# Kernel tuning notes

Hardware: AMD Instinct MI355X
Metric: run time of the kernel (lower is better)

Reference implementation:

```python
import jax, jax.numpy as jnp
import numpy as np

# ---- geometry constants (match init_kwargs) ----
A3, A2, W2D = 180, 128, 384          # cone views, parallel angles, 2D sino detector bins
NV, NU = 192, 256                    # cone detector rows/cols (== 2D BP recon grid)
VZ, VY, VX = 192, 192, 192           # volume shape
DS2D = 2.0                           # 2D sinogram detector spacing
DU, DV = 2.0, 2.0                    # cone detector spacing
VOX = 1.0                            # voxel spacing
DSO, DSD = 750.0, 1200.0             # source-isocenter / source-detector distance


def _grad_last(x):
    """torch.gradient along last axis with unit spacing (central diff, one-sided edges)."""
    left = x[..., 1:2] - x[..., 0:1]
    mid = (x[..., 2:] - x[..., :-2]) * 0.5
    right = x[..., -1:] - x[..., -2:-1]
    return jnp.concatenate([left, mid, right], axis=-1)


def _parallel_bp_2d(sino):
    """Batched 2D parallel-beam backprojection. sino [A3, A2, W2D] -> [A3, NV, NU]."""
    dt = sino.dtype
    thetas = jnp.arange(A2, dtype=dt) * jnp.asarray(np.pi / A2, dt)
    ys = (jnp.arange(NV, dtype=dt) - (NV - 1) / 2.0) * DV   # recon grid = detector plane
    xs = (jnp.arange(NU, dtype=dt) - (NU - 1) / 2.0) * DU
    Yg, Xg = ys[:, None], xs[None, :]

    def body(acc, inp):
        th, s_a = inp                       # s_a: [A3, W2D] (one angle, all views)
        pos = (Xg * jnp.cos(th) + Yg * jnp.sin(th)) / DS2D + (W2D - 1) / 2.0  # [NV,NU]
        i0 = jnp.floor(pos).astype(jnp.int32)
        f = (pos - i0).astype(dt)
        i1 = i0 + 1
        w0 = (1.0 - f) * ((i0 >= 0) & (i0 < W2D)).astype(dt)
        w1 = f * ((i1 >= 0) & (i1 < W2D)).astype(dt)
        i0c = jnp.clip(i0, 0, W2D - 1)
        i1c = jnp.clip(i1, 0, W2D - 1)
        g = s_a[:, i0c] * w0 + s_a[:, i1c] * w1   # [A3, NV, NU]
        return acc + g, None

    acc = jnp.zeros((A3, NV, NU), dt)
    acc, _ = jax.lax.scan(jax.checkpoint(body), acc, (thetas, jnp.swapaxes(sino, 0, 1)))
    return acc * jnp.asarray(np.pi / A2, dt)


def _weights_3d(dt):
    """Cosine detector weight D / sqrt(D^2 + u^2 + v^2), shape [NV, NU]."""
    us = (jnp.arange(NU, dtype=dt) - (NU - 1) / 2.0) * DU
    vs = (jnp.arange(NV, dtype=dt) - (NV - 1) / 2.0) * DV
    return DSD / jnp.sqrt(DSD * DSD + us[None, :] ** 2 + vs[:, None] ** 2)


def _cone_bp_3d(proj):
    """Circular cone-beam backprojection. proj [A3, NV, NU] -> [VZ, VY, VX]."""
    dt = proj.dtype
    betas = jnp.arange(A3, dtype=dt) * jnp.asarray(2.0 * np.pi / A3, dt)
    zs = (jnp.arange(VZ, dtype=dt) - (VZ - 1) / 2.0) * VOX
    ys = (jnp.arange(VY, dtype=dt) - (VY - 1) / 2.0) * VOX
    xs = (jnp.arange(VX, dtype=dt) - (VX - 1) / 2.0) * VOX
    Z, Y, X = zs[:, None, None], ys[None, :, None], xs[None, None, :]

    def body(acc, inp):
        beta, p = inp                                     # p: [NV, NU]
        cb, sb = jnp.cos(beta), jnp.sin(beta)
        r = X * cb + Y * sb                               # toward source
        t = -X * sb + Y * cb                              # detector u direction
        denom = DSO - r                                   # [1,VY,VX] (broadcast)
        iu = (DSD * t / denom) / DU + (NU - 1) / 2.0      # [1,VY,VX]
        iv = (DSD * Z / denom) / DV + (NV - 1) / 2.0      # [VZ,VY,VX]
        i0u = jnp.floor(iu).astype(jnp.int32); fu = (iu - i0u).astype(dt); i1u = i0u + 1
        i0v = jnp.floor(iv).astype(jnp.int32); fv = (iv - i0v).astype(dt); i1v = i0v + 1
        inb = lambda i, n: ((i >= 0) & (i < n)).astype(dt)
        m0u, m1u = inb(i0u, NU), inb(i1u, NU)
        m0v, m1v = inb(i0v, NV), inb(i1v, NV)
        i0uc, i1uc = jnp.clip(i0u, 0, NU - 1), jnp.clip(i1u, 0, NU - 1)
        i0vc, i1vc = jnp.clip(i0v, 0, NV - 1), jnp.clip(i1v, 0, NV - 1)
        val = (p[i0vc, i0uc] * ((1 - fv) * m0v) * ((1 - fu) * m0u)
               + p[i0vc, i1uc] * ((1 - fv) * m0v) * (fu * m1u)
               + p[i1vc, i0uc] * (fv * m1v) * ((1 - fu) * m0u)
               + p[i1vc, i1uc] * (fv * m1v) * (fu * m1u))   # [VZ,VY,VX]
        w = (DSO / denom) ** 2                              # FDK distance weight
        return acc + w * val, None

    acc = jnp.zeros((VZ, VY, VX), dt)
    acc, _ = jax.lax.scan(jax.checkpoint(body), acc, (betas, proj))
    return acc * jnp.asarray(2.0 * np.pi / A3, dt)


def setup_inputs() -> dict:
    key = jax.random.key(0)
    k1, k2 = jax.random.split(key)
    sinogram = jax.random.normal(k1, (1, 1, A3, A2, W2D), dtype=jnp.float32)
    weight_init = jax.random.uniform(k2, (A3, A2, W2D), dtype=jnp.float32)
    return {"sinogram": sinogram, "weight_init": weight_init}


def reference(sinogram, weight_init):
    ws = sinogram[0] * weight_init          # [1, A3, A2, W2D]
    d = _grad_last(ws)[0]                   # gradient along dim=3, squeeze dim 0
    cb = _parallel_bp_2d(d)                 # [A3, NV, NU]
    wcb = cb * _weights_3d(cb.dtype)        # Defrise-Clack detector weighting
    reco = _cone_bp_3d(wcb)                 # [VZ, VY, VX]
    return reco[None]                       # [1, VZ, VY, VX]
```

## Files before the change

kernel.cpp:

```cpp
#include <hip/hip_runtime.h>

#define A3 180
#define A2 128
#define W2D 384
#define NV 192
#define NU 256
#define VZ 192
#define VY 192
#define VX 192

#define BX 32
#define BY 8
#define CZPT 12
#define WROWS 32
#define WDW 64

#define BU2 32
#define BV2 32
#define VPT2 4
#define PW 64

static constexpr double PI_D = 3.14159265358979323846;

typedef float f32x2 __attribute__((ext_vector_type(2)));

#define GLOAD16(gaddr, laddr)                                                    \
    __builtin_amdgcn_global_load_lds(                                            \
        (const __attribute__((address_space(1))) unsigned int*)(gaddr),          \
        (__attribute__((address_space(3))) unsigned int*)(laddr), 16, 0, 0)
#define GLOAD4(gaddr, laddr)                                                     \
    __builtin_amdgcn_global_load_lds(                                            \
        (const __attribute__((address_space(1))) unsigned int*)(gaddr),          \
        (__attribute__((address_space(3))) unsigned int*)(laddr), 4, 0, 0)

__global__ void tables_kernel(float* __restrict__ c2, float* __restrict__ s2,
                              float* __restrict__ cbt, float* __restrict__ sbt) {
    int i = threadIdx.x;
    if (i < A2) {
        float th = (float)i * (float)(PI_D / A2);
        c2[i] = cosf(th);
        s2[i] = sinf(th);
    }
    if (i < A3) {
        float be = (float)i * (float)(2.0 * PI_D / A3);
        cbt[i] = cosf(be);
        sbt[i] = sinf(be);
    }
}

__global__ __launch_bounds__(W2D) void grad_kernel(const float* __restrict__ sino,
                                                   const float* __restrict__ wini,
                                                   float* __restrict__ d) {
    __shared__ float p[W2D];
    size_t base = (size_t)blockIdx.x * W2D;
    int w = threadIdx.x;
    p[w] = sino[base + w] * wini[base + w];
    __syncthreads();
    float g;
    if (w == 0)            g = p[1] - p[0];
    else if (w == W2D - 1) g = p[W2D - 1] - p[W2D - 2];
    else                   g = (p[w + 1] - p[w - 1]) * 0.5f;
    d[base + w] = g;
}

__global__ __launch_bounds__(256) void bp2d_kernel(const float* __restrict__ d,
                                                   const float* __restrict__ c2,
                                                   const float* __restrict__ s2,
                                                   float* __restrict__ wcb) {
    __shared__ float rowwin[2][4][PW];
    __shared__ float csl[A2], ssl[A2];
    __shared__ int umin_s[A2];

    int tid = threadIdx.x;
    int ul = tid & 31;
    int vth = tid >> 5;
    int wv = tid >> 6;
    int lane = tid & 63;
    int u0g = blockIdx.x * BU2;
    int v0g = blockIdx.y * BV2;
    int a3 = blockIdx.z;

    float uf = (float)(u0g + ul) - 127.5f;
    float vf0 = (float)(v0g + vth * VPT2) - 95.5f;
    const float* slab = d + (size_t)a3 * (A2 * W2D);

    if (tid < A2) {
        float c = c2[tid], s = s2[tid];
        csl[tid] = c; ssl[tid] = s;
        float cu0 = ((float)u0g - 127.5f) * c;
        float cu1 = ((float)(u0g + BU2 - 1) - 127.5f) * c;
        float cv0 = ((float)v0g - 95.5f) * s;
        float cv1 = ((float)(v0g + BV2 - 1) - 95.5f) * s;
        float m = fminf(cu0, cu1) + fminf(cv0, cv1) + 191.5f;
        umin_s[tid] = (int)m - 2;
    }
    __syncthreads();

    {
        int um = umin_s[wv];
        int colg = min(um + lane, W2D - 1);
        GLOAD4(slab + wv * W2D + colg, &rowwin[0][wv][0]);
    }
    __syncthreads();

    float acc[VPT2];
#pragma unroll
    for (int k = 0; k < VPT2; ++k) acc[k] = 0.0f;

    for (int g = 0; g < A2 / 4; ++g) {
        int buf = g & 1;
        if (g + 1 < A2 / 4) {
            int aa = (g + 1) * 4 + wv;
            int um = umin_s[aa];
            int colg = min(um + lane, W2D - 1);
            GLOAD4(slab + aa * W2D + colg, &rowwin[buf ^ 1][wv][0]);
        }
#pragma unroll
        for (int j = 0; j < 4; ++j) {
            int aa = g * 4 + j;
            float c = csl[aa], s = ssl[aa];
            float pb = fmaf(uf, c, fmaf(vf0, s, 191.5f - (float)umin_s[aa]));
            const float* rw = rowwin[buf][j];
#pragma unroll
            for (int k = 0; k < VPT2; ++k) {
                float pos = fmaf((float)k, s, pb);
                int i0 = (int)pos;
                float f = __builtin_amdgcn_fractf(pos);
                float r0 = rw[i0], r1 = rw[i0 + 1];
                acc[k] = fmaf(f, r1 - r0, acc[k] + r0);
            }
        }
        __syncthreads();
    }

    float x = uf * 2.0f;
    float scale = (float)((PI_D / A2) * (2.0 * PI_D / A3));
#pragma unroll
    for (int k = 0; k < VPT2; ++k) {
        float y = (vf0 + (float)k) * 2.0f;
        float w3 = 1200.0f * __builtin_amdgcn_rsqf(1440000.0f + x * x + y * y);
        int v = v0g + vth * VPT2 + k;
        wcb[((size_t)a3 * NV + v) * NU + u0g + ul] = acc[k] * scale * w3;
    }
}

__global__ __launch_bounds__(256, 8) void conebp_kernel(const float* __restrict__ wcb,
                                                        const float* __restrict__ cbt,
                                                        const float* __restrict__ sbt,
                                                        float* __restrict__ out) {
    __shared__ float win[2][WROWS * WDW];
    __shared__ int orgs_s[A3 + 2];

    int tid = threadIdx.x;
    int tx = tid & (BX - 1);
    int ty = tid >> 5;
    int wid = tid >> 6;
    int lane = tid & 63;

    int x = blockIdx.x * BX + tx;
    int y = blockIdx.y * BY + ty;
    int z0 = blockIdx.z * CZPT;

    float xf = (float)x - 95.5f;
    float yf = (float)y - 95.5f;
    float z0f = (float)z0 - 95.5f;

    {
        float cxf0 = (float)(blockIdx.x * BX) - 95.5f;
        float cxf1 = cxf0 + (float)(BX - 1);
        float cyf0 = (float)(blockIdx.y * BY) - 95.5f;
        float cyf1 = cyf0 + (float)(BY - 1);
        if (tid < A3) {
            float cbb = cbt[tid], sbb = sbt[tid];
            float iumin = 1e30f, ivmin = 1e30f;
#pragma unroll
            for (int c = 0; c < 4; ++c) {
                float cx = (c & 1) ? cxf1 : cxf0;
                float cy = (c & 2) ? cyf1 : cyf0;
                float rr = cx * cbb + cy * sbb;
                float inv = __builtin_amdgcn_rcpf(750.0f - rr);
                float tt = cy * cbb - cx * sbb;
                iumin = fminf(iumin, fmaf(600.0f * tt, inv, 135.5f));
                ivmin = fminf(ivmin, fmaf(600.0f * z0f, inv, 95.5f));
            }
            int um = (int)iumin - 9;
            um = min(max(um, 0), 192) & ~3;
            int vm = min(max((int)ivmin - 1, 1), 160);
            orgs_s[tid] = (vm << 16) | um;
        }
        if (tid >= A3 && tid < A3 + 2) orgs_s[tid] = (1 << 16);
    }
    __syncthreads();

    f32x2 acc2[CZPT];
#pragma unroll
    for (int k = 0; k < CZPT; ++k) acc2[k] = (f32x2)0.0f;

    unsigned pre = ((unsigned)(lane >> 4) << 8) + ((unsigned)(lane & 15) << 2)
                 + ((unsigned)wid << 10);
    float* const win0 = &win[0][0];
    float* const win1 = &win[1][0];

    int orgc = orgs_s[0];
    int orgn = orgs_s[1];
    {
        unsigned umin = orgc & 0xffffu, vmin = (unsigned)orgc >> 16;
        const float* src = wcb + (vmin << 8) + umin + pre;
        float* dst = win0 + ((unsigned)wid << 8);
        GLOAD16(src, dst);
        GLOAD16(src + 4096, dst + 1024);
    }
    __syncthreads();

    for (int a = 0; a < A3; ++a) {
        int cur = a & 1;

        if (a + 1 < A3) {
            unsigned umin = orgn & 0xffffu, vmin = (unsigned)orgn >> 16;
            const float* src = wcb + (size_t)(a + 1) * (NV * NU)
                             + (vmin << 8) + umin + pre;
            float* dst = (cur ? win0 : win1) + ((unsigned)wid << 8);
            GLOAD16(src, dst);
            GLOAD16(src + 4096, dst + 1024);
        }

        float cb = cbt[a], sb = sbt[a];
        float r = fmaf(xf, cb, yf * sb);
        float t = fmaf(yf, cb, -xf * sb);
        float inv = __builtin_amdgcn_rcpf(750.0f - r);
        float iub = fmaf(600.0f * t, inv, 135.5f);
        int u0 = (int)iub - 8;
        float fu = __builtin_amdgcn_fractf(iub);
        float wgt = 750.0f * inv;
        wgt *= wgt;
        float wa = ((unsigned)u0 < NU) ? (1.0f - fu) * wgt : 0.0f;
        float wb = ((unsigned)(u0 + 1) < NU) ? fu * wgt : 0.0f;
        f32x2 wab; wab.x = wa; wab.y = wb;
        float dstep = 600.0f * inv;

        unsigned uminc = orgc & 0xffffu, vminc = (unsigned)orgc >> 16;
        float ivr = fmaf(dstep, z0f, 95.5f - (float)vminc);
        const float* w0 = (cur ? win1 : win0) + (u0 - (int)uminc);

#pragma unroll
        for (int k = 0; k < CZPT; ++k) {
            float iv = fmaf((float)k, dstep, ivr);
            int v0 = (int)iv;
            float fv = __builtin_amdgcn_fractf(iv);
            int o = v0 << 6;
            f32x2 p0; p0.x = w0[o];       p0.y = w0[o + 1];
            f32x2 p1; p1.x = w0[o + WDW]; p1.y = w0[o + WDW + 1];
            f32x2 fv2; fv2.x = fv; fv2.y = fv;
            f32x2 q = __builtin_elementwise_fma(fv2, p1 - p0, p0);
            acc2[k] = __builtin_elementwise_fma(wab, q, acc2[k]);
        }

        __syncthreads();
        orgc = orgn;
        orgn = orgs_s[a + 2];
    }

#pragma unroll
    for (int k = 0; k < CZPT; ++k) {
        out[(((size_t)(z0 + k)) * VY + y) * VX + x] = acc2[k].x + acc2[k].y;
    }
}

extern "C" void kernel_launch(void* const* d_in, const int* in_sizes, int n_in,
                              void* d_out, int out_size, void* d_ws, size_t ws_size,
                              hipStream_t stream) {
    const float* sino = (const float*)d_in[0];
    const float* wini = (const float*)d_in[1];
    float* out = (float*)d_out;

    float* d   = (float*)d_ws;
    float* wcb = d + (size_t)A3 * A2 * W2D;
    float* c2  = wcb + (size_t)A3 * NV * NU;
    float* s2  = c2 + A2;
    float* cbt = s2 + A2;
    float* sbt = cbt + A3;

    tables_kernel<<<1, 256, 0, stream>>>(c2, s2, cbt, sbt);
    grad_kernel<<<A3 * A2, W2D, 0, stream>>>(sino, wini, d);
    bp2d_kernel<<<dim3(NU / BU2, NV / BV2, A3), 256, 0, stream>>>(d, c2, s2, wcb);
    conebp_kernel<<<dim3(VX / BX, VY / BY, VZ / CZPT), 256, 0, stream>>>(wcb, cbt, sbt, out);
}
```

Measured before the change: 757.4 us.

## Process two projection angles per barrier with four shrunken LDS window buffers

Each per-angle LDS window shrinks from 32 to 20 rows, and the buffer count rises from two to four. The main loop now handles two angles per iteration and prefetches the next pair, which halves the number of __syncthreads barriers. The smaller window keeps total LDS roughly constant and lowers load traffic, since the second 16-byte load is issued only by wave 0. The risk is that 20 rows may not cover the vertical footprint of all 12 z-slices at every angle, which could read outside the staged rows.

```diff
diff --git a/kernel.cpp b/kernel.cpp
--- a/kernel.cpp
+++ b/kernel.cpp
@@ -12,7 +12,7 @@
 #define BX 32
 #define BY 8
 #define CZPT 12
-#define WROWS 32
+#define WROWS 20
 #define WDW 64
 
 #define BU2 32
@@ -148,8 +148,8 @@
                                                         const float* __restrict__ cbt,
                                                         const float* __restrict__ sbt,
                                                         float* __restrict__ out) {
-    __shared__ float win[2][WROWS * WDW];
-    __shared__ int orgs_s[A3 + 2];
+    __shared__ float win[4][WROWS * WDW];
+    __shared__ int orgs_s[A3];
 
     int tid = threadIdx.x;
     int tx = tid & (BX - 1);
@@ -185,10 +185,9 @@
             }
             int um = (int)iumin - 9;
             um = min(max(um, 0), 192) & ~3;
-            int vm = min(max((int)ivmin - 1, 1), 160);
+            int vm = min(max((int)ivmin - 1, 1), 172);
             orgs_s[tid] = (vm << 16) | um;
         }
-        if (tid >= A3 && tid < A3 + 2) orgs_s[tid] = (1 << 16);
     }
     __syncthreads();
 
@@ -198,33 +197,19 @@
 
     unsigned pre = ((unsigned)(lane >> 4) << 8) + ((unsigned)(lane & 15) << 2)
                  + ((unsigned)wid << 10);
-    float* const win0 = &win[0][0];
-    float* const win1 = &win[1][0];
-
-    int orgc = orgs_s[0];
-    int orgn = orgs_s[1];
-    {
-        unsigned umin = orgc & 0xffffu, vmin = (unsigned)orgc >> 16;
-        const float* src = wcb + (vmin << 8) + umin + pre;
-        float* dst = win0 + ((unsigned)wid << 8);
-        GLOAD16(src, dst);
-        GLOAD16(src + 4096, dst + 1024);
-    }
-    __syncthreads();
-
-    for (int a = 0; a < A3; ++a) {
-        int cur = a & 1;
-
-        if (a + 1 < A3) {
-            unsigned umin = orgn & 0xffffu, vmin = (unsigned)orgn >> 16;
-            const float* src = wcb + (size_t)(a + 1) * (NV * NU)
-                             + (vmin << 8) + umin + pre;
-            float* dst = (cur ? win0 : win1) + ((unsigned)wid << 8);
-            GLOAD16(src, dst);
-            GLOAD16(src + 4096, dst + 1024);
-        }
-
-        float cb = cbt[a], sb = sbt[a];
+
+    auto stage = [&](int b, int buf) {
+        int org = orgs_s[b];
+        unsigned umin = org & 0xffffu, vmin = (unsigned)org >> 16;
+        const float* src = wcb + (size_t)b * (NV * NU) + (vmin << 8) + umin;
+        float* dst = &win[buf][0];
+        GLOAD16(src + pre, dst + ((unsigned)wid << 8));
+        if (wid == 0)
+            GLOAD16(src + 4096 + pre, dst + 1024);
+    };
+
+    auto compute = [&](int b, int buf) {
+        float cb = cbt[b], sb = sbt[b];
         float r = fmaf(xf, cb, yf * sb);
         float t = fmaf(yf, cb, -xf * sb);
         float inv = __builtin_amdgcn_rcpf(750.0f - r);
@@ -238,9 +223,10 @@
         f32x2 wab; wab.x = wa; wab.y = wb;
         float dstep = 600.0f * inv;
 
-        unsigned uminc = orgc & 0xffffu, vminc = (unsigned)orgc >> 16;
+        int org = orgs_s[b];
+        unsigned uminc = org & 0xffffu, vminc = (unsigned)org >> 16;
         float ivr = fmaf(dstep, z0f, 95.5f - (float)vminc);
-        const float* w0 = (cur ? win1 : win0) + (u0 - (int)uminc);
+        const float* w0 = &win[buf][0] + (u0 - (int)uminc);
 
 #pragma unroll
         for (int k = 0; k < CZPT; ++k) {
@@ -254,10 +240,21 @@
             f32x2 q = __builtin_elementwise_fma(fv2, p1 - p0, p0);
             acc2[k] = __builtin_elementwise_fma(wab, q, acc2[k]);
         }
-
+    };
+
+    stage(0, 0);
+    stage(1, 1);
+    __syncthreads();
+
+    for (int p = 0; p < A3 / 2; ++p) {
+        int cur = (p & 1) << 1;
+        if (p + 1 < A3 / 2) {
+            stage(2 * p + 2, cur ^ 2);
+            stage(2 * p + 3, (cur ^ 2) + 1);
+        }
+        compute(2 * p,     cur);
+        compute(2 * p + 1, cur + 1);
         __syncthreads();
-        orgc = orgn;
-        orgn = orgs_s[a + 2];
     }
 
 #pragma unroll
```

New measurement: 735.0 us. 3.0% less time.
